# Performance work log

Measured on AMD Instinct MI355X. Metric: run time of the kernel, lower is better.

## Reference

```python
import jax, jax.numpy as jnp
import numpy as np

B = 2_097_152          # batch of theta samples
POLY_DEG = 127         # QSP polynomial degree -> 128 phases
PI = np.float32(np.pi)


def setup_inputs() -> dict:
    key = jax.random.key(0)
    k1, k2 = jax.random.split(key)
    th = jax.random.uniform(k1, (B, 1), dtype=jnp.float32) * PI
    phis = jax.random.uniform(k2, (POLY_DEG + 1, 1), dtype=jnp.float32) * PI
    return {"th": th, "phis": phis}


def reference(th, phis):
    # th: [B,1] float32, phis: [P+1,1] float32 (learned QSP phases)
    theta = th[:, 0]                      # [B]
    c = jnp.cos(theta)
    s = jnp.sin(theta)
    # expm(i*theta*X) = cos(theta) I + i sin(theta) X  (closed form, no expm)
    wx = jnp.stack(
        [jnp.stack([c + 0j, 1j * s], axis=-1),
         jnp.stack([1j * s, c + 0j], axis=-1)],
        axis=-2,
    ).astype(jnp.complex64)               # [B,2,2]

    phi = phis[:, 0]                      # [P+1]
    e = jnp.exp(1j * phi).astype(jnp.complex64)
    # expm(i*phi*Z) = diag(e^{i phi}, e^{-i phi})
    rz = (jnp.zeros((phi.shape[0], 2, 2), jnp.complex64)
          .at[:, 0, 0].set(e)
          .at[:, 1, 1].set(jnp.conj(e)))  # [P+1,2,2]

    u0 = jnp.broadcast_to(rz[0], (theta.shape[0], 2, 2))  # [B,2,2]

    def step(u, rzk):
        u = jnp.einsum('bij,bjk->bik', u, wx)   # u @ W(x)
        u = jnp.einsum('bij,jk->bik', u, rzk)   # ... @ Rz(phi_k)
        return u, None

    u, _ = jax.lax.scan(step, u0, rz[1:])       # 127 sequential steps
    # convention == 0: (Re[u_00], Im[u_00])
    return (jnp.real(u[:, 0, 0]), jnp.imag(u[:, 0, 0]))
```

## Files before the change

kernel.cpp:

```cpp
#include <hip/hip_runtime.h>


typedef float v2f __attribute__((ext_vector_type(2)));

#define NPHI 128

__device__ __forceinline__ float wave_shr1(float x) {
    return __builtin_bit_cast(float,
        __builtin_amdgcn_update_dpp(0, __builtin_bit_cast(int, x),
                                    0x138, 0xf, 0xf, true));
}

__global__ __launch_bounds__(512, 4) void qsp_fused(
    const float* __restrict__ th,
    const float* __restrict__ phis,
    float* __restrict__ out,
    int Bq8)
{
    __shared__ alignas(16) float2 g2[NPHI];
    __shared__ float2 h[NPHI];

    const int tid = threadIdx.x;

    if (tid < 64) {
        const int L = tid;
        float sp, cp;
        __sincosf(phis[L], &sp, &cp);
        h[L] = make_float2(0.5f * cp, 0.5f * sp);
        __sincosf(phis[L + 64], &sp, &cp);
        h[L + 64] = make_float2(0.5f * cp, 0.5f * sp);

        v2f A0 = {0.f, 0.f}, B0 = {0.f, 0.f};
        v2f A1 = {0.f, 0.f}, B1 = {0.f, 0.f};
        const float2 h0 = h[0];
        if (L == 0) A0 = (v2f){2.f * h0.x, 2.f * h0.y};

        #pragma unroll 4
        for (int k = 1; k < NPHI; ++k) {
            const float2 hk = h[k];
            const v2f hx  = {hk.x, hk.x};
            const v2f hyn = {-hk.y, hk.y};
            const v2f hyp = {hk.y, -hk.y};
            const v2f pA = { wave_shr1(A1.x), wave_shr1(A1.y) };
            const v2f pB = { wave_shr1(B1.x), wave_shr1(B1.y) };
            const v2f u0 = pA + pB, v0 = A0 - B0;
            const v2f sA0 = u0 + v0, sB0 = u0 - v0;
            const v2f u1 = A0 + B0, v1 = A1 - B1;
            const v2f sA1 = u1 + v1, sB1 = u1 - v1;
            v2f ts;
            ts = (v2f){sA0.y, sA0.x};
            A0 = __builtin_elementwise_fma(hyn, ts, hx * sA0);
            ts = (v2f){sB0.y, sB0.x};
            B0 = __builtin_elementwise_fma(hyp, ts, hx * sB0);
            ts = (v2f){sA1.y, sA1.x};
            A1 = __builtin_elementwise_fma(hyn, ts, hx * sA1);
            ts = (v2f){sB1.y, sB1.x};
            B1 = __builtin_elementwise_fma(hyp, ts, hx * sB1);
        }
        g2[2 * L]     = make_float2(A0.x, A0.y);
        g2[2 * L + 1] = make_float2(A1.x, A1.y);
    }

    const int idx = blockIdx.x * blockDim.x + tid;
    const int lidx = (idx < Bq8) ? idx : 0;
    const float4 ta = ((const float4*)th)[2 * lidx];
    const float4 tb = ((const float4*)th)[2 * lidx + 1];
    const float th8[8] = {ta.x, ta.y, ta.z, ta.w, tb.x, tb.y, tb.z, tb.w};

    v2f zr[4], zi[4], nzi[4], Cc[4], Ss[4];
    #pragma unroll
    for (int g = 0; g < 4; ++g) {
        float s0, c0, s1, c1;
        __sincosf(2.f * th8[2 * g],     &s0, &c0);
        __sincosf(2.f * th8[2 * g + 1], &s1, &c1);
        zr[g]  = (v2f){c0, c1};
        zi[g]  = (v2f){s0, s1};
        nzi[g] = (v2f){-s0, -s1};
        __sincosf(127.f * th8[2 * g],     &s0, &c0);
        __sincosf(127.f * th8[2 * g + 1], &s1, &c1);
        Cc[g] = (v2f){c0, c1};
        Ss[g] = (v2f){s0, s1};
    }

    __syncthreads();

    v2f ar[4] = {{0.f,0.f},{0.f,0.f},{0.f,0.f},{0.f,0.f}};
    v2f ai[4] = {{0.f,0.f},{0.f,0.f},{0.f,0.f},{0.f,0.f}};
    const float4* g4 = (const float4*)g2;

    #pragma unroll 4
    for (int jj = NPHI / 2 - 1; jj >= 0; --jj) {
        const float4 gp = g4[jj];
        {
            const v2f gr = {gp.z, gp.z}, gi = {gp.w, gp.w};
            #pragma unroll
            for (int g = 0; g < 4; ++g) {
                const v2f nr = __builtin_elementwise_fma(
                    ar[g], zr[g], __builtin_elementwise_fma(ai[g], nzi[g], gr));
                const v2f ni = __builtin_elementwise_fma(
                    ar[g], zi[g], __builtin_elementwise_fma(ai[g], zr[g], gi));
                ar[g] = nr; ai[g] = ni;
            }
        }
        {
            const v2f gr = {gp.x, gp.x}, gi = {gp.y, gp.y};
            #pragma unroll
            for (int g = 0; g < 4; ++g) {
                const v2f nr = __builtin_elementwise_fma(
                    ar[g], zr[g], __builtin_elementwise_fma(ai[g], nzi[g], gr));
                const v2f ni = __builtin_elementwise_fma(
                    ar[g], zi[g], __builtin_elementwise_fma(ai[g], zr[g], gi));
                ar[g] = nr; ai[g] = ni;
            }
        }
    }

    v2f orv[4], oiv[4];
    #pragma unroll
    for (int g = 0; g < 4; ++g) {
        orv[g] = __builtin_elementwise_fma(ar[g], Cc[g], ai[g] * Ss[g]);
        oiv[g] = __builtin_elementwise_fma(ai[g], Cc[g], -(ar[g] * Ss[g]));
    }

    if (idx < Bq8) {
        float4* o4 = (float4*)out;
        const int ib = 2 * Bq8;
        o4[2 * idx]          = make_float4(orv[0].x, orv[0].y, orv[1].x, orv[1].y);
        o4[2 * idx + 1]      = make_float4(orv[2].x, orv[2].y, orv[3].x, orv[3].y);
        o4[ib + 2 * idx]     = make_float4(oiv[0].x, oiv[0].y, oiv[1].x, oiv[1].y);
        o4[ib + 2 * idx + 1] = make_float4(oiv[2].x, oiv[2].y, oiv[3].x, oiv[3].y);
    }
}

extern "C" void kernel_launch(void* const* d_in, const int* in_sizes, int n_in,
                              void* d_out, int out_size, void* d_ws, size_t ws_size,
                              hipStream_t stream)
{
    const float* th   = (const float*)d_in[0];
    const float* phis = (const float*)d_in[1];
    float* out = (float*)d_out;
    const int B = in_sizes[0];
    const int Bq8 = B >> 3;
    const int block = 512;
    const int grid = (Bq8 + block - 1) / block;
    qsp_fused<<<grid, block, 0, stream>>>(th, phis, out, Bq8);
}
```

Baseline: 88.12 us.

## Scalarize QSP kernel, halve block size, prefetch LDS coefficients, defer sincos

Replaces the packed two-wide float vectors with scalar fp32 math in both the phase-polynomial precompute and the per-sample Horner loop. The block size drops from 512 to 256, which doubles the number of blocks that each redo the per-block 64-thread coefficient precompute. The LDS coefficient load is software-prefetched one iteration ahead. The 127*theta sincos moves to the epilogue so fewer registers stay live. The intent is to cut register pressure and improve latency hiding, at the cost of giving up packed-FMA throughput and repeating the serial precompute more often.

New measurement: 87.83 us. About the same (-0.3%).

```diff
diff --git a/kernel.cpp b/kernel.cpp
--- a/kernel.cpp
+++ b/kernel.cpp
@@ -1,7 +1,5 @@
 #include <hip/hip_runtime.h>
 
-
-typedef float v2f __attribute__((ext_vector_type(2)));
 
 #define NPHI 128
 
@@ -11,7 +9,7 @@
                                     0x138, 0xf, 0xf, true));
 }
 
-__global__ __launch_bounds__(512, 4) void qsp_fused(
+__global__ __launch_bounds__(256, 4) void qsp_fused(
     const float* __restrict__ th,
     const float* __restrict__ phis,
     float* __restrict__ out,
@@ -30,35 +28,35 @@
         __sincosf(phis[L + 64], &sp, &cp);
         h[L + 64] = make_float2(0.5f * cp, 0.5f * sp);
 
-        v2f A0 = {0.f, 0.f}, B0 = {0.f, 0.f};
-        v2f A1 = {0.f, 0.f}, B1 = {0.f, 0.f};
+        float A0r = 0.f, A0i = 0.f, B0r = 0.f, B0i = 0.f;
+        float A1r = 0.f, A1i = 0.f, B1r = 0.f, B1i = 0.f;
         const float2 h0 = h[0];
-        if (L == 0) A0 = (v2f){2.f * h0.x, 2.f * h0.y};
+        if (L == 0) { A0r = 2.f * h0.x; A0i = 2.f * h0.y; }
 
         #pragma unroll 4
         for (int k = 1; k < NPHI; ++k) {
             const float2 hk = h[k];
-            const v2f hx  = {hk.x, hk.x};
-            const v2f hyn = {-hk.y, hk.y};
-            const v2f hyp = {hk.y, -hk.y};
-            const v2f pA = { wave_shr1(A1.x), wave_shr1(A1.y) };
-            const v2f pB = { wave_shr1(B1.x), wave_shr1(B1.y) };
-            const v2f u0 = pA + pB, v0 = A0 - B0;
-            const v2f sA0 = u0 + v0, sB0 = u0 - v0;
-            const v2f u1 = A0 + B0, v1 = A1 - B1;
-            const v2f sA1 = u1 + v1, sB1 = u1 - v1;
-            v2f ts;
-            ts = (v2f){sA0.y, sA0.x};
-            A0 = __builtin_elementwise_fma(hyn, ts, hx * sA0);
-            ts = (v2f){sB0.y, sB0.x};
-            B0 = __builtin_elementwise_fma(hyp, ts, hx * sB0);
-            ts = (v2f){sA1.y, sA1.x};
-            A1 = __builtin_elementwise_fma(hyn, ts, hx * sA1);
-            ts = (v2f){sB1.y, sB1.x};
-            B1 = __builtin_elementwise_fma(hyp, ts, hx * sB1);
+            const float hx = hk.x, hy = hk.y;
+            const float pAr = wave_shr1(A1r), pAi = wave_shr1(A1i);
+            const float pBr = wave_shr1(B1r), pBi = wave_shr1(B1i);
+            const float u0r = pAr + pBr, u0i = pAi + pBi;
+            const float v0r = A0r - B0r, v0i = A0i - B0i;
+            const float sA0r = u0r + v0r, sA0i = u0i + v0i;
+            const float sB0r = u0r - v0r, sB0i = u0i - v0i;
+            const float u1r = A0r + B0r, u1i = A0i + B0i;
+            const float v1r = A1r - B1r, v1i = A1i - B1i;
+            const float sA1r = u1r + v1r, sA1i = u1i + v1i;
+            const float sB1r = u1r - v1r, sB1i = u1i - v1i;
+            A0r = fmaf(hx, sA0r, -hy * sA0i);
+            A0i = fmaf(hx, sA0i,  hy * sA0r);
+            B0r = fmaf(hx, sB0r,  hy * sB0i);
+            B0i = fmaf(hx, sB0i, -hy * sB0r);
+            A1r = fmaf(hx, sA1r, -hy * sA1i);
+            A1i = fmaf(hx, sA1i,  hy * sA1r);
+            B1r = fmaf(hx, sB1r,  hy * sB1i);
+            B1i = fmaf(hx, sB1i, -hy * sB1r);
         }
-        g2[2 * L]     = make_float2(A0.x, A0.y);
-        g2[2 * L + 1] = make_float2(A1.x, A1.y);
+        ((float4*)g2)[L] = make_float4(A0r, A0i, A1r, A1i);
     }
 
     const int idx = blockIdx.x * blockDim.x + tid;
@@ -67,68 +65,69 @@
     const float4 tb = ((const float4*)th)[2 * lidx + 1];
     const float th8[8] = {ta.x, ta.y, ta.z, ta.w, tb.x, tb.y, tb.z, tb.w};
 
-    v2f zr[4], zi[4], nzi[4], Cc[4], Ss[4];
+    float zr[8], zi[8];
     #pragma unroll
-    for (int g = 0; g < 4; ++g) {
-        float s0, c0, s1, c1;
-        __sincosf(2.f * th8[2 * g],     &s0, &c0);
-        __sincosf(2.f * th8[2 * g + 1], &s1, &c1);
-        zr[g]  = (v2f){c0, c1};
-        zi[g]  = (v2f){s0, s1};
-        nzi[g] = (v2f){-s0, -s1};
-        __sincosf(127.f * th8[2 * g],     &s0, &c0);
-        __sincosf(127.f * th8[2 * g + 1], &s1, &c1);
-        Cc[g] = (v2f){c0, c1};
-        Ss[g] = (v2f){s0, s1};
+    for (int e = 0; e < 8; ++e) {
+        float s, c;
+        __sincosf(2.f * th8[e], &s, &c);
+        zr[e] = c; zi[e] = s;
     }
 
     __syncthreads();
 
-    v2f ar[4] = {{0.f,0.f},{0.f,0.f},{0.f,0.f},{0.f,0.f}};
-    v2f ai[4] = {{0.f,0.f},{0.f,0.f},{0.f,0.f},{0.f,0.f}};
+    float ar[8], ai[8];
+    #pragma unroll
+    for (int e = 0; e < 8; ++e) { ar[e] = 0.f; ai[e] = 0.f; }
+
     const float4* g4 = (const float4*)g2;
+    float4 gp = g4[NPHI / 2 - 1];
 
     #pragma unroll 4
-    for (int jj = NPHI / 2 - 1; jj >= 0; --jj) {
-        const float4 gp = g4[jj];
-        {
-            const v2f gr = {gp.z, gp.z}, gi = {gp.w, gp.w};
-            #pragma unroll
-            for (int g = 0; g < 4; ++g) {
-                const v2f nr = __builtin_elementwise_fma(
-                    ar[g], zr[g], __builtin_elementwise_fma(ai[g], nzi[g], gr));
-                const v2f ni = __builtin_elementwise_fma(
-                    ar[g], zi[g], __builtin_elementwise_fma(ai[g], zr[g], gi));
-                ar[g] = nr; ai[g] = ni;
-            }
+    for (int jj = NPHI / 2 - 1; jj >= 1; --jj) {
+        const float4 gn = g4[jj - 1];
+        #pragma unroll
+        for (int e = 0; e < 8; ++e) {
+            const float nr = fmaf(ar[e], zr[e], fmaf(-ai[e], zi[e], gp.z));
+            const float ni = fmaf(ar[e], zi[e], fmaf( ai[e], zr[e], gp.w));
+            ar[e] = nr; ai[e] = ni;
         }
-        {
-            const v2f gr = {gp.x, gp.x}, gi = {gp.y, gp.y};
-            #pragma unroll
-            for (int g = 0; g < 4; ++g) {
-                const v2f nr = __builtin_elementwise_fma(
-                    ar[g], zr[g], __builtin_elementwise_fma(ai[g], nzi[g], gr));
-                const v2f ni = __builtin_elementwise_fma(
-                    ar[g], zi[g], __builtin_elementwise_fma(ai[g], zr[g], gi));
-                ar[g] = nr; ai[g] = ni;
-            }
+        #pragma unroll
+        for (int e = 0; e < 8; ++e) {
+            const float nr = fmaf(ar[e], zr[e], fmaf(-ai[e], zi[e], gp.x));
+            const float ni = fmaf(ar[e], zi[e], fmaf( ai[e], zr[e], gp.y));
+            ar[e] = nr; ai[e] = ni;
         }
+        gp = gn;
+    }
+    #pragma unroll
+    for (int e = 0; e < 8; ++e) {
+        const float nr = fmaf(ar[e], zr[e], fmaf(-ai[e], zi[e], gp.z));
+        const float ni = fmaf(ar[e], zi[e], fmaf( ai[e], zr[e], gp.w));
+        ar[e] = nr; ai[e] = ni;
+    }
+    #pragma unroll
+    for (int e = 0; e < 8; ++e) {
+        const float nr = fmaf(ar[e], zr[e], fmaf(-ai[e], zi[e], gp.x));
+        const float ni = fmaf(ar[e], zi[e], fmaf( ai[e], zr[e], gp.y));
+        ar[e] = nr; ai[e] = ni;
     }
 
-    v2f orv[4], oiv[4];
+    float orv[8], oiv[8];
     #pragma unroll
-    for (int g = 0; g < 4; ++g) {
-        orv[g] = __builtin_elementwise_fma(ar[g], Cc[g], ai[g] * Ss[g]);
-        oiv[g] = __builtin_elementwise_fma(ai[g], Cc[g], -(ar[g] * Ss[g]));
+    for (int e = 0; e < 8; ++e) {
+        float S, C;
+        __sincosf(127.f * th8[e], &S, &C);
+        orv[e] = fmaf(ar[e], C,  ai[e] * S);
+        oiv[e] = fmaf(ai[e], C, -ar[e] * S);
     }
 
     if (idx < Bq8) {
         float4* o4 = (float4*)out;
         const int ib = 2 * Bq8;
-        o4[2 * idx]          = make_float4(orv[0].x, orv[0].y, orv[1].x, orv[1].y);
-        o4[2 * idx + 1]      = make_float4(orv[2].x, orv[2].y, orv[3].x, orv[3].y);
-        o4[ib + 2 * idx]     = make_float4(oiv[0].x, oiv[0].y, oiv[1].x, oiv[1].y);
-        o4[ib + 2 * idx + 1] = make_float4(oiv[2].x, oiv[2].y, oiv[3].x, oiv[3].y);
+        o4[2 * idx]          = make_float4(orv[0], orv[1], orv[2], orv[3]);
+        o4[2 * idx + 1]      = make_float4(orv[4], orv[5], orv[6], orv[7]);
+        o4[ib + 2 * idx]     = make_float4(oiv[0], oiv[1], oiv[2], oiv[3]);
+        o4[ib + 2 * idx + 1] = make_float4(oiv[4], oiv[5], oiv[6], oiv[7]);
     }
 }
 
@@ -141,7 +140,7 @@
     float* out = (float*)d_out;
     const int B = in_sizes[0];
     const int Bq8 = B >> 3;
-    const int block = 512;
+    const int block = 256;
     const int grid = (Bq8 + block - 1) / block;
     qsp_fused<<<grid, block, 0, stream>>>(th, phis, out, Bq8);
 }
```
